# Kernel tuning notes

Measured on AMD Instinct MI355X. Metric: run time of the kernel, lower is better.

The kernel has to match this reference:

```python
import jax, jax.numpy as jnp
import numpy as np

C = 256
G = 32  # groups
EPS = 1e-5

def _xavier(key, shape, gain=1.0):
    fan_in, fan_out = shape[1], shape[0]
    a = gain * np.sqrt(6.0 / (fan_in + fan_out))
    return jax.random.uniform(key, shape, jnp.float32, -a, a)

def setup_inputs() -> dict:
    key = jax.random.key(0)
    ks = jax.random.split(key, 5)
    x = jax.random.normal(ks[0], (2, C, 16, 16, 16), jnp.float32)
    return {
        "x": x,
        "gn_gamma": jnp.ones((C,), jnp.float32),
        "gn_beta": jnp.zeros((C,), jnp.float32),
        "Wq": _xavier(ks[1], (C, C)), "bq": jnp.zeros((C,), jnp.float32),
        "Wk": _xavier(ks[2], (C, C)), "bk": jnp.zeros((C,), jnp.float32),
        "Wv": _xavier(ks[3], (C, C)), "bv": jnp.zeros((C,), jnp.float32),
        "Wp": _xavier(ks[4], (C, C), gain=1e-05), "bp": jnp.zeros((C,), jnp.float32),
    }

def reference(x, gn_gamma, gn_beta, Wq, bq, Wk, bk, Wv, bv, Wp, bp):
    B, Cc, D, H, W = x.shape
    N = D * H * W
    xf = x.reshape(B, Cc, N)  # [B, C, N]
    # GroupNorm over (C//G, N) per group
    xg = xf.reshape(B, G, Cc // G, N)
    mu = jnp.mean(xg, axis=(2, 3), keepdims=True)
    var = jnp.var(xg, axis=(2, 3), keepdims=True)
    h = ((xg - mu) * jax.lax.rsqrt(var + EPS)).reshape(B, Cc, N)
    h = h * gn_gamma[None, :, None] + gn_beta[None, :, None]
    # 1x1x1 convs == channel matmuls
    q = jnp.einsum('oc,bcn->bno', Wq, h) + bq  # [B, N, C]
    k = jnp.einsum('oc,bcn->bon', Wk, h) + bk[None, :, None]  # [B, C, N]
    v = jnp.einsum('oc,bcn->bno', Wv, h) + bv  # [B, N, C]
    scale = float(Cc) ** (-0.5)
    w = jnp.einsum('bnc,bcm->bnm', q, k) * scale  # [B, N, N]
    w = jax.nn.softmax(w, axis=-1)
    a = jnp.einsum('bnm,bmc->bnc', w, v)  # [B, N, C]
    out = jnp.einsum('oc,bnc->bon', Wp, a) + bp[None, :, None]  # [B, C, N]
    return x + out.reshape(B, Cc, D, H, W)
```

## Files before the change

### kernel.cpp

```cpp
#include <hip/hip_runtime.h>
#include <stdint.h>

#define B_ 2
#define C_ 256
#define N_ 4096
#define EPS_ 1e-5f

typedef short short8 __attribute__((ext_vector_type(8)));
typedef float f32x4 __attribute__((ext_vector_type(4)));
typedef float f32x16 __attribute__((ext_vector_type(16)));
typedef long long i64;

static __device__ __forceinline__ unsigned short f2bf(float f) {
    union { float f; unsigned int u; } v; v.f = f;
    unsigned int r = v.u + 0x7FFF + ((v.u >> 16) & 1);
    return (unsigned short)(r >> 16);
}
static __device__ __forceinline__ float bf2f(unsigned short u) {
    union { unsigned int u; float f; } v; v.u = ((unsigned int)u) << 16;
    return v.f;
}
static __device__ __forceinline__ unsigned char f2fp8(float f) {
    return (unsigned char)(__builtin_amdgcn_cvt_pk_fp8_f32(f, f, 0, false) & 0xff);
}
static __device__ __forceinline__ unsigned short pk_bf8(float a, float b) {
    return (unsigned short)(__builtin_amdgcn_cvt_pk_bf8_f32(a, b, 0, false) & 0xffff);
}

__global__ __launch_bounds__(256) void prep(
    const float* __restrict__ x, float2* __restrict__ stats,
    const float* __restrict__ Wq, const float* __restrict__ Wk,
    const float* __restrict__ Wv, const float* __restrict__ Wp,
    ushort* __restrict__ o)
{
    __shared__ float as_[4], as2_[4];
    if (blockIdx.x < 64) {
        const float4* p = reinterpret_cast<const float4*>(x + (size_t)blockIdx.x * 32768);
        float s = 0.f, ss = 0.f;
        for (int i = threadIdx.x; i < 8192; i += 256) {
            float4 v = p[i];
            s  += v.x + v.y + v.z + v.w;
            ss += v.x*v.x + v.y*v.y + v.z*v.z + v.w*v.w;
        }
        for (int m = 32; m; m >>= 1) { s += __shfl_down(s, m, 64); ss += __shfl_down(ss, m, 64); }
        int w = threadIdx.x >> 6;
        if ((threadIdx.x & 63) == 0) { as_[w] = s; as2_[w] = ss; }
        __syncthreads();
        if (threadIdx.x == 0) {
            float S = as_[0]+as_[1]+as_[2]+as_[3], SS = as2_[0]+as2_[1]+as2_[2]+as2_[3];
            float mu = S / 32768.f;
            float var = SS / 32768.f - mu*mu;
            stats[blockIdx.x] = make_float2(mu, rsqrtf(var + EPS_));
        }
    } else {
        int t = (blockIdx.x - 64) * 256 + threadIdx.x;
        int idx = t * 4;
        int sel = idx >> 16;
        const float* src = sel == 0 ? Wq : sel == 1 ? Wk : sel == 2 ? Wv : Wp;
        float4 v = *reinterpret_cast<const float4*>(src + (idx & 65535));
        ushort4 r; r.x = f2bf(v.x); r.y = f2bf(v.y); r.z = f2bf(v.z); r.w = f2bf(v.w);
        *reinterpret_cast<ushort4*>(o + idx) = r;
    }
}

__global__ void gnorm_t(const float* __restrict__ x, const float2* __restrict__ stats,
                        const float* __restrict__ gamma, const float* __restrict__ beta,
                        ushort* __restrict__ ht) {
    __shared__ float tile[32][33];
    int b = blockIdx.z, n0 = blockIdx.x * 32, c0 = blockIdx.y * 32;
    int tx = threadIdx.x, ty = threadIdx.y;
    #pragma unroll
    for (int i = 0; i < 4; i++) {
        int c = c0 + ty + i*8;
        float2 st = stats[b*32 + (c >> 3)];
        float v = x[((size_t)(b*C_ + c))*N_ + n0 + tx];
        tile[ty + i*8][tx] = (v - st.x) * st.y * gamma[c] + beta[c];
    }
    __syncthreads();
    #pragma unroll
    for (int i = 0; i < 4; i++) {
        int n = n0 + ty + i*8;
        ht[((size_t)(b*N_ + n))*C_ + c0 + tx] = f2bf(tile[tx][ty + i*8]);
    }
}

__global__ __launch_bounds__(256) void qkvproj(
    const ushort* __restrict__ ht, const ushort* __restrict__ wq,
    const ushort* __restrict__ wk, const ushort* __restrict__ wv,
    const float* __restrict__ bq, const float* __restrict__ bk, const float* __restrict__ bv,
    unsigned char* __restrict__ qo, unsigned char* __restrict__ ko, unsigned char* __restrict__ vo)
{
    __shared__ ushort sA[64][72], sBq[64][72], sBk[64][72], sBv[64][72];
    int bz = blockIdx.z;
    const ushort* Ab = ht + (size_t)bz * N_ * C_;
    int i0 = blockIdx.x * 64, j0 = blockIdx.y * 64;
    int tid = threadIdx.x, w = tid >> 6, lane = tid & 63, lr = lane & 15, lg = lane >> 4;
    f32x4 aq[4] = {}, ak[4] = {}, av[4] = {};
    for (int ks = 0; ks < 256; ks += 64) {
        #pragma unroll
        for (int it = 0; it < 2; it++) {
            int ch = tid + it*256;
            int row = ch >> 3, cc = ch & 7;
            *reinterpret_cast<uint4*>(&sA[row][cc*8]) =
                *reinterpret_cast<const uint4*>(Ab + ((size_t)(i0 + row))*256 + ks + cc*8);
            *reinterpret_cast<uint4*>(&sBq[row][cc*8]) =
                *reinterpret_cast<const uint4*>(wq + ((size_t)(j0 + row))*256 + ks + cc*8);
            *reinterpret_cast<uint4*>(&sBk[row][cc*8]) =
                *reinterpret_cast<const uint4*>(wk + ((size_t)(j0 + row))*256 + ks + cc*8);
            *reinterpret_cast<uint4*>(&sBv[row][cc*8]) =
                *reinterpret_cast<const uint4*>(wv + ((size_t)(j0 + row))*256 + ks + cc*8);
        }
        __syncthreads();
        #pragma unroll
        for (int kc = 0; kc < 2; kc++) {
            short8 af = *reinterpret_cast<const short8*>(&sA[w*16 + lr][kc*32 + lg*8]);
            #pragma unroll
            for (int cb = 0; cb < 4; cb++) {
                short8 b1 = *reinterpret_cast<const short8*>(&sBq[cb*16 + lr][kc*32 + lg*8]);
                short8 b2 = *reinterpret_cast<const short8*>(&sBk[cb*16 + lr][kc*32 + lg*8]);
                short8 b3 = *reinterpret_cast<const short8*>(&sBv[cb*16 + lr][kc*32 + lg*8]);
                aq[cb] = __builtin_amdgcn_mfma_f32_16x16x32_bf16(af, b1, aq[cb], 0, 0, 0);
                ak[cb] = __builtin_amdgcn_mfma_f32_16x16x32_bf16(af, b2, ak[cb], 0, 0, 0);
                av[cb] = __builtin_amdgcn_mfma_f32_16x16x32_bf16(af, b3, av[cb], 0, 0, 0);
            }
        }
        __syncthreads();
    }
    #pragma unroll
    for (int cb = 0; cb < 4; cb++) {
        #pragma unroll
        for (int r = 0; r < 4; r++) {
            int i = i0 + w*16 + lg*4 + r;
            int j = j0 + cb*16 + lr;
            size_t oidx = ((size_t)(bz*N_ + i))*256 + j;
            qo[oidx] = f2fp8(aq[cb][r] + bq[j]);
            ko[oidx] = f2fp8(ak[cb][r] + bk[j]);
            int m = i & 63;
            int col = (i & ~63) + ((m & 31)*2 + (m >> 5));
            vo[((size_t)bz*C_ + j)*N_ + col] = f2fp8(av[cb][r] + bv[j]);
        }
    }
}

#define FLASH_LDS 79872
__global__ __launch_bounds__(256, 2) void flash5(
    const unsigned char* __restrict__ q, const unsigned char* __restrict__ k,
    const unsigned char* __restrict__ vT,
    ushort* __restrict__ Opart, float* __restrict__ lsum, ushort* __restrict__ aout, int nsplit)
{
    extern __shared__ char smem[];
    int b = blockIdx.z, s = blockIdx.y, qt = blockIdx.x;
    int tid = threadIdx.x, w = tid >> 6, lane = tid & 63;
    int l31 = lane & 31, hi = lane >> 5;
    int nrow0 = qt*128 + w*32;
    const unsigned char* kB = k  + (size_t)b * N_ * 256;
    const unsigned char* vB = vT + (size_t)b * 256 * N_;

    i64 qf[16];
    #pragma unroll
    for (int kc = 0; kc < 16; kc++)
        qf[kc] = *reinterpret_cast<const i64*>(
            q + ((size_t)(b*N_) + nrow0 + l31)*256 + kc*16 + hi*8);

    f32x16 oacc[8] = {};
    float lpart[16] = {};

    int tiles = 64 / nsplit;
    int t0 = s * tiles;

    char* kbuf0 = smem;
    char* vbuf0 = smem + 33792;
    char* pw    = smem + 70656 + w*2304;

    uint4 kreg[4], vreg[4];
    auto loadKV = [&](int t) {
        #pragma unroll
        for (int i = 0; i < 4; i++) {
            int row = w*16 + i*4 + (lane >> 4);
            kreg[i] = *reinterpret_cast<const uint4*>(
                kB + (size_t)(t*64 + row)*256 + (lane & 15)*16);
        }
        #pragma unroll
        for (int i = 0; i < 4; i++) {
            int c = w*64 + i*16 + (lane >> 2);
            vreg[i] = *reinterpret_cast<const uint4*>(
                vB + (size_t)c*4096 + t*64 + (lane & 3)*16);
        }
    };
    auto writeKV = [&](int sel) {
        #pragma unroll
        for (int i = 0; i < 4; i++) {
            int row = w*16 + i*4 + (lane >> 4);
            char* p = kbuf0 + sel*16896 + row*264 + (lane & 15)*16;
            *reinterpret_cast<uint2*>(p)     = make_uint2(kreg[i].x, kreg[i].y);
            *reinterpret_cast<uint2*>(p + 8) = make_uint2(kreg[i].z, kreg[i].w);
        }
        #pragma unroll
        for (int i = 0; i < 4; i++) {
            int c = w*64 + i*16 + (lane >> 2);
            char* p = vbuf0 + sel*18432 + c*72 + (lane & 3)*16;
            *reinterpret_cast<uint2*>(p)     = make_uint2(vreg[i].x, vreg[i].y);
            *reinterpret_cast<uint2*>(p + 8) = make_uint2(vreg[i].z, vreg[i].w);
        }
    };

    loadKV(t0);
    writeKV(0);
    __syncthreads();
    int sel = 0;

    for (int ti = 0; ti < tiles; ti++) {
        int t = t0 + ti;
        int tn = (ti + 1 < tiles) ? t + 1 : t0;
        loadKV(tn);

        const char* kb_ = kbuf0 + sel*16896;
        f32x16 s0 = {}, s1 = {};
        __builtin_amdgcn_s_setprio(1);
        #pragma unroll
        for (int kc = 0; kc < 16; kc++) {
            i64 b0 = *reinterpret_cast<const i64*>(kb_ + l31*264        + kc*16 + hi*8);
            i64 b1 = *reinterpret_cast<const i64*>(kb_ + (l31+32)*264   + kc*16 + hi*8);
            s0 = __builtin_amdgcn_mfma_f32_32x32x16_fp8_fp8(qf[kc], b0, s0, 0, 0, 0);
            s1 = __builtin_amdgcn_mfma_f32_32x32x16_fp8_fp8(qf[kc], b1, s1, 0, 0, 0);
        }
        __builtin_amdgcn_s_setprio(0);

        #pragma unroll
        for (int r = 0; r < 16; r++) {
            int R = (r & 3) + 8*(r >> 2) + 4*hi;
            float p0 = __expf(fminf(s0[r]*0.0625f, 10.5f));
            float p1 = __expf(fminf(s1[r]*0.0625f, 10.5f));
            lpart[r] += p0 + p1;
            *(ushort*)(pw + R*72 + l31*2) = pk_bf8(p0, p1);
        }

        const char* vb_ = vbuf0 + sel*18432;
        i64 pa[4];
        #pragma unroll
        for (int ks = 0; ks < 4; ks++)
            pa[ks] = *reinterpret_cast<const i64*>(pw + l31*72 + ks*16 + hi*8);
        __builtin_amdgcn_s_setprio(1);
        #pragma unroll
        for (int cb = 0; cb < 8; cb++) {
            #pragma unroll
            for (int ks = 0; ks < 4; ks++) {
                i64 bv = *reinterpret_cast<const i64*>(vb_ + (cb*32 + l31)*72 + ks*16 + hi*8);
                oacc[cb] = __builtin_amdgcn_mfma_f32_32x32x16_bf8_fp8(pa[ks], bv, oacc[cb], 0, 0, 0);
            }
        }
        __builtin_amdgcn_s_setprio(0);

        writeKV(sel ^ 1);
        __syncthreads();
        sel ^= 1;
    }

    #pragma unroll
    for (int r = 0; r < 16; r++) {
        float v = lpart[r];
        v += __shfl_xor(v, 1, 64);
        v += __shfl_xor(v, 2, 64);
        v += __shfl_xor(v, 4, 64);
        v += __shfl_xor(v, 8, 64);
        v += __shfl_xor(v, 16, 64);
        lpart[r] = v;
    }

    if (nsplit == 1) {
        #pragma unroll
        for (int r = 0; r < 16; r++) {
            int R = (r & 3) + 8*(r >> 2) + 4*hi;
            float inv = 1.f / lpart[r];
            #pragma unroll
            for (int cb = 0; cb < 8; cb++)
                aout[((size_t)(b*N_) + nrow0 + R)*256 + cb*32 + l31] = f2bf(oacc[cb][r] * inv);
        }
    } else {
        size_t obase = ((size_t)(b*nsplit + s)*N_ + nrow0) * 256;
        #pragma unroll
        for (int r = 0; r < 16; r++) {
            int R = (r & 3) + 8*(r >> 2) + 4*hi;
            #pragma unroll
            for (int cb = 0; cb < 8; cb++)
                Opart[obase + (size_t)R*256 + cb*32 + l31] = f2bf(oacc[cb][r]);
        }
        if (l31 == 0) {
            #pragma unroll
            for (int r = 0; r < 16; r++)
                lsum[(size_t)(b*nsplit + s)*N_ + nrow0 + (r & 3) + 8*(r >> 2) + 4*hi] = lpart[r];
        }
    }
}

__global__ void combine2(const ushort* __restrict__ Opart, const float* __restrict__ lsum,
                         ushort* __restrict__ aout, int nsplit) {
    int g = threadIdx.x >> 6, lane = threadIdx.x & 63;
    int idx = blockIdx.x*4 + g;
    int b = idx >> 12, n = idx & 4095;
    float L = 0.f;
    for (int s2 = 0; s2 < nsplit; s2++) L += lsum[(size_t)(b*nsplit + s2)*N_ + n];
    float inv = 1.f / L;
    float a0 = 0.f, a1 = 0.f, a2 = 0.f, a3 = 0.f;
    for (int s2 = 0; s2 < nsplit; s2++) {
        ushort4 o = *reinterpret_cast<const ushort4*>(
            Opart + ((size_t)(b*nsplit + s2)*N_ + n)*256 + lane*4);
        a0 += bf2f(o.x); a1 += bf2f(o.y); a2 += bf2f(o.z); a3 += bf2f(o.w);
    }
    ushort4 r; r.x = f2bf(a0*inv); r.y = f2bf(a1*inv); r.z = f2bf(a2*inv); r.w = f2bf(a3*inv);
    *reinterpret_cast<ushort4*>(aout + (size_t)idx*256 + lane*4) = r;
}

__global__ __launch_bounds__(256) void pgemm(
    const ushort* __restrict__ A, const ushort* __restrict__ Bm,
    const float* __restrict__ bias, const float* __restrict__ resid,
    float* __restrict__ outp, long bBatch, long oBatch)
{
    __shared__ ushort sA[64][72];
    __shared__ ushort sB[64][72];
    int bz = blockIdx.z;
    const ushort* Bb = Bm + (size_t)bBatch * bz;
    int i0 = blockIdx.x * 64, j0 = blockIdx.y * 64;
    int tid = threadIdx.x, w = tid >> 6, lane = tid & 63, lr = lane & 15, lg = lane >> 4;
    f32x4 acc[4] = {};
    for (int ks = 0; ks < 256; ks += 64) {
        #pragma unroll
        for (int it = 0; it < 2; it++) {
            int ch = tid + it*256;
            int row = ch >> 3, cc = ch & 7;
            *reinterpret_cast<uint4*>(&sA[row][cc*8]) =
                *reinterpret_cast<const uint4*>(A + ((size_t)(i0 + row))*256 + ks + cc*8);
            *reinterpret_cast<uint4*>(&sB[row][cc*8]) =
                *reinterpret_cast<const uint4*>(Bb + ((size_t)(j0 + row))*256 + ks + cc*8);
        }
        __syncthreads();
        #pragma unroll
        for (int kc = 0; kc < 2; kc++) {
            short8 af = *reinterpret_cast<const short8*>(&sA[w*16 + lr][kc*32 + lg*8]);
            #pragma unroll
            for (int cb = 0; cb < 4; cb++) {
                short8 bf = *reinterpret_cast<const short8*>(&sB[cb*16 + lr][kc*32 + lg*8]);
                acc[cb] = __builtin_amdgcn_mfma_f32_16x16x32_bf16(af, bf, acc[cb], 0, 0, 0);
            }
        }
        __syncthreads();
    }
    #pragma unroll
    for (int cb = 0; cb < 4; cb++) {
        #pragma unroll
        for (int r = 0; r < 4; r++) {
            int i = i0 + w*16 + lg*4 + r;
            int j = j0 + cb*16 + lr;
            size_t oidx = (size_t)oBatch*bz + (size_t)i*N_ + j;
            outp[oidx] = acc[cb][r] + bias[i] + resid[oidx];
        }
    }
}

extern "C" void kernel_launch(void* const* d_in, const int* in_sizes, int n_in,
                              void* d_out, int out_size, void* d_ws, size_t ws_size,
                              hipStream_t stream) {
    const float* x     = (const float*)d_in[0];
    const float* gamma = (const float*)d_in[1];
    const float* beta  = (const float*)d_in[2];
    const float* Wq = (const float*)d_in[3]; const float* bq = (const float*)d_in[4];
    const float* Wk = (const float*)d_in[5]; const float* bk = (const float*)d_in[6];
    const float* Wv = (const float*)d_in[7]; const float* bv = (const float*)d_in[8];
    const float* Wp = (const float*)d_in[9]; const float* bp = (const float*)d_in[10];
    float* out = (float*)d_out;

    char* ws = (char*)d_ws;
    float2* stats = (float2*)ws;
    ushort* wqb = (ushort*)(ws + 1024);
    ushort* wkb = wqb + 65536;
    ushort* wvb = wkb + 65536;
    ushort* wpb = wvb + 65536;
    ushort* ht  = (ushort*)(ws + 1024 + 524288);
    const size_t NB = (size_t)B_ * N_ * C_;
    unsigned char* qb  = (unsigned char*)(ht + NB);
    unsigned char* kb8 = qb  + NB;
    unsigned char* vTb = kb8 + NB;
    ushort* ab = (ushort*)(vTb + NB);
    char* after = (char*)(ab + NB);
    float*  lsum  = (float*)after;
    ushort* Opart = (ushort*)(after + 262144);

    int nsplit = (ws_size >= (size_t)48*1024*1024) ? 8 : 4;

    hipFuncSetAttribute((const void*)flash5, hipFuncAttributeMaxDynamicSharedMemorySize,
                        FLASH_LDS);

    prep<<<320, 256, 0, stream>>>(x, stats, Wq, Wk, Wv, Wp, wqb);
    gnorm_t<<<dim3(128, 8, 2), dim3(32, 8), 0, stream>>>(x, stats, gamma, beta, ht);
    qkvproj<<<dim3(64, 4, 2), 256, 0, stream>>>(ht, wqb, wkb, wvb, bq, bk, bv, qb, kb8, vTb);
    flash5<<<dim3(32, nsplit, 2), 256, FLASH_LDS, stream>>>(qb, kb8, vTb, Opart, lsum, ab, nsplit);
    combine2<<<2048, 256, 0, stream>>>(Opart, lsum, ab, nsplit);
    pgemm<<<dim3(4, 64, 2), 256, 0, stream>>>(wpb, ab, bp, x, out, (long)N_*C_, (long)C_*N_);
}
```

Measured before the change: 84.47 us.

## Compute S transposed so P stays in registers, dropping the LDS round trip

The QK^T MFMA now swaps its operands to produce S^T, so each lane holds a contiguous run of keys for one query row. The exp values are packed four at a time into bf8 and exchanged across the half-waves with shuffles to form the P operand directly, which removes the per-wave P staging buffer in LDS and its write/read traffic. The V-transpose column permutation in qkvproj is dropped to match the new register layout, row sums collapse to a single scalar per lane, and K/V load addresses are precomputed and advanced incrementally with the redundant final prefetch skipped. The risk is that any mismatch between the shuffle-based P layout and the V layout would silently corrupt the attention output.

```diff
diff --git a/kernel.cpp b/kernel.cpp
--- a/kernel.cpp
+++ b/kernel.cpp
@@ -23,8 +23,13 @@
 static __device__ __forceinline__ unsigned char f2fp8(float f) {
     return (unsigned char)(__builtin_amdgcn_cvt_pk_fp8_f32(f, f, 0, false) & 0xff);
 }
-static __device__ __forceinline__ unsigned short pk_bf8(float a, float b) {
-    return (unsigned short)(__builtin_amdgcn_cvt_pk_bf8_f32(a, b, 0, false) & 0xffff);
+static __device__ __forceinline__ unsigned int pack4_bf8(float a, float b, float c, float d) {
+    int v = __builtin_amdgcn_cvt_pk_bf8_f32(a, b, 0, false);
+    v = __builtin_amdgcn_cvt_pk_bf8_f32(c, d, v, true);
+    return (unsigned int)v;
+}
+static __device__ __forceinline__ i64 mk64(unsigned int lo, unsigned int hi) {
+    return (i64)(((unsigned long long)hi << 32) | (unsigned long long)lo);
 }
 
 __global__ __launch_bounds__(256) void prep(
@@ -135,15 +140,13 @@
             size_t oidx = ((size_t)(bz*N_ + i))*256 + j;
             qo[oidx] = f2fp8(aq[cb][r] + bq[j]);
             ko[oidx] = f2fp8(ak[cb][r] + bk[j]);
-            int m = i & 63;
-            int col = (i & ~63) + ((m & 31)*2 + (m >> 5));
-            vo[((size_t)bz*C_ + j)*N_ + col] = f2fp8(av[cb][r] + bv[j]);
-        }
-    }
-}
-
-#define FLASH_LDS 79872
-__global__ __launch_bounds__(256, 2) void flash5(
+            vo[((size_t)bz*C_ + j)*N_ + i] = f2fp8(av[cb][r] + bv[j]);
+        }
+    }
+}
+
+#define FLASH_LDS 70656
+__global__ __launch_bounds__(256, 2) void flash10(
     const unsigned char* __restrict__ q, const unsigned char* __restrict__ k,
     const unsigned char* __restrict__ vT,
     ushort* __restrict__ Opart, float* __restrict__ lsum, ushort* __restrict__ aout, int nsplit)
@@ -163,115 +166,124 @@
             q + ((size_t)(b*N_) + nrow0 + l31)*256 + kc*16 + hi*8);
 
     f32x16 oacc[8] = {};
-    float lpart[16] = {};
+    float lp = 0.f;
 
     int tiles = 64 / nsplit;
     int t0 = s * tiles;
 
     char* kbuf0 = smem;
     char* vbuf0 = smem + 33792;
-    char* pw    = smem + 70656 + w*2304;
+
+    int koff[4], kd[4], voff[4], vd[4];
+    #pragma unroll
+    for (int i = 0; i < 4; i++) {
+        int row = w*16 + i*4 + (lane >> 4);
+        koff[i] = (t0*64 + row)*256 + (lane & 15)*16;
+        kd[i]   = row*264 + (lane & 15)*16;
+        int c = w*64 + i*16 + (lane >> 2);
+        voff[i] = c*4096 + t0*64 + (lane & 3)*16;
+        vd[i]   = c*72 + (lane & 3)*16;
+    }
 
     uint4 kreg[4], vreg[4];
-    auto loadKV = [&](int t) {
-        #pragma unroll
-        for (int i = 0; i < 4; i++) {
-            int row = w*16 + i*4 + (lane >> 4);
-            kreg[i] = *reinterpret_cast<const uint4*>(
-                kB + (size_t)(t*64 + row)*256 + (lane & 15)*16);
-        }
-        #pragma unroll
-        for (int i = 0; i < 4; i++) {
-            int c = w*64 + i*16 + (lane >> 2);
-            vreg[i] = *reinterpret_cast<const uint4*>(
-                vB + (size_t)c*4096 + t*64 + (lane & 3)*16);
-        }
+    auto loadKV = [&]() {
+        #pragma unroll
+        for (int i = 0; i < 4; i++) { kreg[i] = *reinterpret_cast<const uint4*>(kB + koff[i]); koff[i] += 16384; }
+        #pragma unroll
+        for (int i = 0; i < 4; i++) { vreg[i] = *reinterpret_cast<const uint4*>(vB + voff[i]); voff[i] += 64; }
     };
     auto writeKV = [&](int sel) {
         #pragma unroll
         for (int i = 0; i < 4; i++) {
-            int row = w*16 + i*4 + (lane >> 4);
-            char* p = kbuf0 + sel*16896 + row*264 + (lane & 15)*16;
+            char* p = kbuf0 + sel*16896 + kd[i];
             *reinterpret_cast<uint2*>(p)     = make_uint2(kreg[i].x, kreg[i].y);
             *reinterpret_cast<uint2*>(p + 8) = make_uint2(kreg[i].z, kreg[i].w);
         }
         #pragma unroll
         for (int i = 0; i < 4; i++) {
-            int c = w*64 + i*16 + (lane >> 2);
-            char* p = vbuf0 + sel*18432 + c*72 + (lane & 3)*16;
+            char* p = vbuf0 + sel*18432 + vd[i];
             *reinterpret_cast<uint2*>(p)     = make_uint2(vreg[i].x, vreg[i].y);
             *reinterpret_cast<uint2*>(p + 8) = make_uint2(vreg[i].z, vreg[i].w);
         }
     };
 
-    loadKV(t0);
+    loadKV();
     writeKV(0);
     __syncthreads();
     int sel = 0;
 
     for (int ti = 0; ti < tiles; ti++) {
-        int t = t0 + ti;
-        int tn = (ti + 1 < tiles) ? t + 1 : t0;
-        loadKV(tn);
+        bool more = (ti + 1 < tiles);
+        if (more) loadKV();
 
         const char* kb_ = kbuf0 + sel*16896;
         f32x16 s0 = {}, s1 = {};
         __builtin_amdgcn_s_setprio(1);
         #pragma unroll
         for (int kc = 0; kc < 16; kc++) {
-            i64 b0 = *reinterpret_cast<const i64*>(kb_ + l31*264        + kc*16 + hi*8);
-            i64 b1 = *reinterpret_cast<const i64*>(kb_ + (l31+32)*264   + kc*16 + hi*8);
-            s0 = __builtin_amdgcn_mfma_f32_32x32x16_fp8_fp8(qf[kc], b0, s0, 0, 0, 0);
-            s1 = __builtin_amdgcn_mfma_f32_32x32x16_fp8_fp8(qf[kc], b1, s1, 0, 0, 0);
+            i64 ka0 = *reinterpret_cast<const i64*>(kb_ + l31*264        + kc*16 + hi*8);
+            i64 ka1 = *reinterpret_cast<const i64*>(kb_ + (l31+32)*264   + kc*16 + hi*8);
+            s0 = __builtin_amdgcn_mfma_f32_32x32x16_fp8_fp8(ka0, qf[kc], s0, 0, 0, 0);
+            s1 = __builtin_amdgcn_mfma_f32_32x32x16_fp8_fp8(ka1, qf[kc], s1, 0, 0, 0);
         }
         __builtin_amdgcn_s_setprio(0);
 
+        float e0[16], e1[16];
+        #pragma unroll
+        for (int r = 0; r < 16; r++) {
+            e0[r] = __expf(fminf(s0[r]*0.0625f, 10.5f));
+            e1[r] = __expf(fminf(s1[r]*0.0625f, 10.5f));
+            lp += e0[r] + e1[r];
+        }
+        unsigned p0 = pack4_bf8(e0[0],e0[1],e0[2],e0[3]);
+        unsigned p1 = pack4_bf8(e0[4],e0[5],e0[6],e0[7]);
+        unsigned p2 = pack4_bf8(e0[8],e0[9],e0[10],e0[11]);
+        unsigned p3 = pack4_bf8(e0[12],e0[13],e0[14],e0[15]);
+        unsigned t0_ = pack4_bf8(e1[0],e1[1],e1[2],e1[3]);
+        unsigned t1_ = pack4_bf8(e1[4],e1[5],e1[6],e1[7]);
+        unsigned t2_ = pack4_bf8(e1[8],e1[9],e1[10],e1[11]);
+        unsigned t3_ = pack4_bf8(e1[12],e1[13],e1[14],e1[15]);
+        unsigned xp0 = (unsigned)__shfl_xor((int)p0, 32, 64);
+        unsigned xp1 = (unsigned)__shfl_xor((int)p1, 32, 64);
+        unsigned xp2 = (unsigned)__shfl_xor((int)p2, 32, 64);
+        unsigned xp3 = (unsigned)__shfl_xor((int)p3, 32, 64);
+        unsigned xt0 = (unsigned)__shfl_xor((int)t0_, 32, 64);
+        unsigned xt1 = (unsigned)__shfl_xor((int)t1_, 32, 64);
+        unsigned xt2 = (unsigned)__shfl_xor((int)t2_, 32, 64);
+        unsigned xt3 = (unsigned)__shfl_xor((int)t3_, 32, 64);
+        i64 A0 = mk64(hi ? xp1 : p0,  hi ? p1 : xp0);
+        i64 A1 = mk64(hi ? xp3 : p2,  hi ? p3 : xp2);
+        i64 A2 = mk64(hi ? xt1 : t0_, hi ? t1_ : xt0);
+        i64 A3 = mk64(hi ? xt3 : t2_, hi ? t3_ : xt2);
+
+        const char* vb_ = vbuf0 + sel*18432;
+        __builtin_amdgcn_s_setprio(1);
+        #pragma unroll
+        for (int cb = 0; cb < 8; cb++) {
+            const char* vrow = vb_ + (cb*32 + l31)*72;
+            i64 bv0 = *reinterpret_cast<const i64*>(vrow + 0*16  + hi*8);
+            oacc[cb] = __builtin_amdgcn_mfma_f32_32x32x16_bf8_fp8(A0, bv0, oacc[cb], 0, 0, 0);
+            i64 bv1 = *reinterpret_cast<const i64*>(vrow + 1*16  + hi*8);
+            oacc[cb] = __builtin_amdgcn_mfma_f32_32x32x16_bf8_fp8(A1, bv1, oacc[cb], 0, 0, 0);
+            i64 bv2 = *reinterpret_cast<const i64*>(vrow + 2*16  + hi*8);
+            oacc[cb] = __builtin_amdgcn_mfma_f32_32x32x16_bf8_fp8(A2, bv2, oacc[cb], 0, 0, 0);
+            i64 bv3 = *reinterpret_cast<const i64*>(vrow + 3*16  + hi*8);
+            oacc[cb] = __builtin_amdgcn_mfma_f32_32x32x16_bf8_fp8(A3, bv3, oacc[cb], 0, 0, 0);
+        }
+        __builtin_amdgcn_s_setprio(0);
+
+        if (more) writeKV(sel ^ 1);
+        __syncthreads();
+        sel ^= 1;
+    }
+
+    lp += __shfl_xor(lp, 32, 64);
+
+    if (nsplit == 1) {
+        float inv = 1.f / lp;
         #pragma unroll
         for (int r = 0; r < 16; r++) {
             int R = (r & 3) + 8*(r >> 2) + 4*hi;
-            float p0 = __expf(fminf(s0[r]*0.0625f, 10.5f));
-            float p1 = __expf(fminf(s1[r]*0.0625f, 10.5f));
-            lpart[r] += p0 + p1;
-            *(ushort*)(pw + R*72 + l31*2) = pk_bf8(p0, p1);
-        }
-
-        const char* vb_ = vbuf0 + sel*18432;
-        i64 pa[4];
-        #pragma unroll
-        for (int ks = 0; ks < 4; ks++)
-            pa[ks] = *reinterpret_cast<const i64*>(pw + l31*72 + ks*16 + hi*8);
-        __builtin_amdgcn_s_setprio(1);
-        #pragma unroll
-        for (int cb = 0; cb < 8; cb++) {
-            #pragma unroll
-            for (int ks = 0; ks < 4; ks++) {
-                i64 bv = *reinterpret_cast<const i64*>(vb_ + (cb*32 + l31)*72 + ks*16 + hi*8);
-                oacc[cb] = __builtin_amdgcn_mfma_f32_32x32x16_bf8_fp8(pa[ks], bv, oacc[cb], 0, 0, 0);
-            }
-        }
-        __builtin_amdgcn_s_setprio(0);
-
-        writeKV(sel ^ 1);
-        __syncthreads();
-        sel ^= 1;
-    }
-
-    #pragma unroll
-    for (int r = 0; r < 16; r++) {
-        float v = lpart[r];
-        v += __shfl_xor(v, 1, 64);
-        v += __shfl_xor(v, 2, 64);
-        v += __shfl_xor(v, 4, 64);
-        v += __shfl_xor(v, 8, 64);
-        v += __shfl_xor(v, 16, 64);
-        lpart[r] = v;
-    }
-
-    if (nsplit == 1) {
-        #pragma unroll
-        for (int r = 0; r < 16; r++) {
-            int R = (r & 3) + 8*(r >> 2) + 4*hi;
-            float inv = 1.f / lpart[r];
             #pragma unroll
             for (int cb = 0; cb < 8; cb++)
                 aout[((size_t)(b*N_) + nrow0 + R)*256 + cb*32 + l31] = f2bf(oacc[cb][r] * inv);
@@ -285,11 +297,8 @@
             for (int cb = 0; cb < 8; cb++)
                 Opart[obase + (size_t)R*256 + cb*32 + l31] = f2bf(oacc[cb][r]);
         }
-        if (l31 == 0) {
-            #pragma unroll
-            for (int r = 0; r < 16; r++)
-                lsum[(size_t)(b*nsplit + s)*N_ + nrow0 + (r & 3) + 8*(r >> 2) + 4*hi] = lpart[r];
-        }
+        if (hi == 0)
+            lsum[(size_t)(b*nsplit + s)*N_ + nrow0 + l31] = lp;
     }
 }
 
@@ -387,13 +396,13 @@
 
     int nsplit = (ws_size >= (size_t)48*1024*1024) ? 8 : 4;
 
-    hipFuncSetAttribute((const void*)flash5, hipFuncAttributeMaxDynamicSharedMemorySize,
+    hipFuncSetAttribute((const void*)flash10, hipFuncAttributeMaxDynamicSharedMemorySize,
                         FLASH_LDS);
 
     prep<<<320, 256, 0, stream>>>(x, stats, Wq, Wk, Wv, Wp, wqb);
     gnorm_t<<<dim3(128, 8, 2), dim3(32, 8), 0, stream>>>(x, stats, gamma, beta, ht);
     qkvproj<<<dim3(64, 4, 2), 256, 0, stream>>>(ht, wqb, wkb, wvb, bq, bk, bv, qb, kb8, vTb);
-    flash5<<<dim3(32, nsplit, 2), 256, FLASH_LDS, stream>>>(qb, kb8, vTb, Opart, lsum, ab, nsplit);
+    flash10<<<dim3(32, nsplit, 2), 256, FLASH_LDS, stream>>>(qb, kb8, vTb, Opart, lsum, ab, nsplit);
     combine2<<<2048, 256, 0, stream>>>(Opart, lsum, ab, nsplit);
     pgemm<<<dim3(4, 64, 2), 256, 0, stream>>>(wpb, ab, bp, x, out, (long)N_*C_, (long)C_*N_);
 }
```

Result: slower. 87.48 us (+3.6%).
